# Optimization experiments

Hardware: AMD Instinct MI355X
Metric: run time of the kernel (lower is better)

Reference implementation:

```python
import jax, jax.numpy as jnp
import numpy as np

B, C1, C2, H, W = 4, 128, 256, 128, 128
K, S = 3, 1
N = K * K  # num sampled points = 9
BN_EPS = 1e-5


def setup_inputs() -> dict:
    key = jax.random.key(0)
    ks = jax.random.split(key, 8)
    x = jax.random.normal(ks[0], (B, C1, H, W), jnp.float32)
    # offset-prediction conv: 3x3, stride S, pad 1, out channels 2*N
    w_off = jax.random.normal(ks[1], (2 * N, C1, 3, 3), jnp.float32) * 0.01
    b_off = jnp.zeros((2 * N,), jnp.float32)
    # main conv over the N sampled points: equivalent to Conv2d(C1,C2,(N,1),stride=(N,1),bias=None)
    w_main = jax.random.normal(ks[2], (C2, C1, N), jnp.float32) * (1.0 / np.sqrt(C1 * N))
    bn_gamma = jax.random.uniform(ks[3], (C2,), jnp.float32, 0.5, 1.5)
    bn_beta = jax.random.normal(ks[4], (C2,), jnp.float32) * 0.1
    bn_mean = jax.random.normal(ks[5], (C2,), jnp.float32) * 0.1
    bn_var = jax.random.uniform(ks[6], (C2,), jnp.float32, 0.5, 1.5)
    return dict(x=x, w_off=w_off, b_off=b_off, w_main=w_main,
                bn_gamma=bn_gamma, bn_beta=bn_beta, bn_mean=bn_mean, bn_var=bn_var)


def _grid_pn():
    # base kernel sampling grid for N points: round(sqrt(N)) x base grid, values 0..base-1
    base = int(round(np.sqrt(N)))
    px, py = np.meshgrid(np.arange(base), np.arange(base), indexing='ij')
    return jnp.asarray(px.reshape(-1), jnp.float32), jnp.asarray(py.reshape(-1), jnp.float32)


def _akconv_forward(x, w_off, b_off, w_main, bn_gamma, bn_beta, bn_mean, bn_var):
    # offset prediction: (b, 2N, h, w)
    offset = jax.lax.conv_general_dilated(
        x, w_off, (S, S), ((1, 1), (1, 1)),
        dimension_numbers=('NCHW', 'OIHW', 'NCHW')) + b_off[None, :, None, None]
    b, _, h, w = offset.shape
    off_x = offset[:, :N].transpose(0, 2, 3, 1)   # (b,h,w,N) row offsets
    off_y = offset[:, N:].transpose(0, 2, 3, 1)   # (b,h,w,N) col offsets
    pn_x, pn_y = _grid_pn()
    p0_x = (jnp.arange(h, dtype=jnp.float32) * S)[None, :, None, None]
    p0_y = (jnp.arange(w, dtype=jnp.float32) * S)[None, None, :, None]
    px = jnp.clip(off_x + pn_x[None, None, None, :] + p0_x, 0.0, H - 1.0)
    py = jnp.clip(off_y + pn_y[None, None, None, :] + p0_y, 0.0, W - 1.0)
    x0 = jnp.clip(jnp.floor(px), 0.0, H - 1.0)
    y0 = jnp.clip(jnp.floor(py), 0.0, W - 1.0)
    x1 = jnp.clip(x0 + 1.0, 0.0, H - 1.0)
    y1 = jnp.clip(y0 + 1.0, 0.0, W - 1.0)
    # bilinear weights (official AKConv formulation)
    g_lt = (1.0 + (x0 - px)) * (1.0 + (y0 - py))
    g_rb = (1.0 - (x1 - px)) * (1.0 - (y1 - py))
    g_lb = (1.0 + (x0 - px)) * (1.0 - (y1 - py))
    g_rt = (1.0 - (x1 - px)) * (1.0 + (y0 - py))
    xf = x.reshape(b, C1, H * W)

    def gather(qx, qy):
        idx = (qx * W + qy).astype(jnp.int32).reshape(b, 1, h * w * N)
        g = jnp.take_along_axis(xf, jnp.broadcast_to(idx, (b, C1, h * w * N)), axis=2)
        return g.reshape(b, C1, h, w, N)

    # fused bilinear combine: (b, C1, h, w, N)
    x_off = (g_lt[:, None] * gather(x0, y0)
             + g_rb[:, None] * gather(x1, y1)
             + g_lb[:, None] * gather(x0, y1)
             + g_rt[:, None] * gather(x1, y0))
    # main conv over sampled points == Conv2d(kernel=(N,1), stride=(N,1)) on rearranged tensor
    out = jnp.einsum('bchwn,ocn->bohw', x_off, w_main)
    # inference-mode BatchNorm
    inv = bn_gamma / jnp.sqrt(bn_var + BN_EPS)
    out = out * inv[None, :, None, None] + (bn_beta - bn_mean * inv)[None, :, None, None]
    # wrapper SiLU activation
    return jax.nn.silu(out)


def reference(x, w_off, b_off, w_main, bn_gamma, bn_beta, bn_mean, bn_var):
    return _akconv_forward(x, w_off, b_off, w_main, bn_gamma, bn_beta, bn_mean, bn_var)
```

## Files before the change

kernel.cpp:

```cpp
#include <hip/hip_runtime.h>
#include <math.h>

typedef __attribute__((ext_vector_type(8))) short short8;
typedef __attribute__((ext_vector_type(4))) float f32x4;
typedef __attribute__((ext_vector_type(2))) float f32x2;
typedef __attribute__((ext_vector_type(4))) uint  uint4v;
typedef __attribute__((ext_vector_type(4))) int   int4v;

#define BB  4
#define C1  128
#define C2  256
#define HH  128
#define WW  128
#define NPT 9
#define HWN (HH*WW)

#define XT_OFF    0ull
#define WB3_OFF   16777216ull
#define BN_OFF    (WB3_OFF + 589824ull)
#define OFFP_OFF  (BN_OFF + 2048ull)
#define PART_OFF  (OFFP_OFF + 4718592ull)
#define WS_FUSED_NEED (PART_OFF + 18874368ull)

#define NB_OFF  (4 * BB * HH)
#define NB_TR   (BB * 4 * HH * 2)
#define NB_PREP 1153

__device__ __forceinline__ ushort f2bf(float f) {
  uint u = __builtin_bit_cast(uint, f);
  u += 0x7FFFu + ((u >> 16) & 1u);
  return (ushort)(u >> 16);
}
__device__ __forceinline__ float u2f(uint u) {
  return __builtin_bit_cast(float, u);
}

__global__ __launch_bounds__(256) void stage1(
    const float* __restrict__ x, const float* __restrict__ b_off,
    const float* __restrict__ w_off, const float* __restrict__ w_main,
    const float* __restrict__ g, const float* __restrict__ be,
    const float* __restrict__ mu, const float* __restrict__ var,
    ushort* ws_u, float* ws_f, float* __restrict__ part) {
  __shared__ __align__(16) ushort tile[32][68];
  int blk = blockIdx.x;
  int tid = threadIdx.x;

  if (blk < NB_OFF) {
    int cg = blk & 3, bh = blk >> 2;
    int h = bh & 127, b = bh >> 7;
    int w = tid & 127, q = tid >> 7;
    int qu = __builtin_amdgcn_readfirstlane(q);
    int quoff = qu * 9;
    const float* xb = x + ((size_t)b * C1 + cg * 32) * HWN;

    f32x2 acc2[9];
    float accs[9];
#pragma unroll
    for (int i = 0; i < 9; ++i) {
      acc2[i] = (f32x2)0.0f;
      accs[i] = (cg == 0) ? b_off[quoff + i] : 0.f;
    }

    int hc0 = (h >= 1) ? h - 1 : 0, hc2 = (h < 127) ? h + 1 : 127;
    int wc0 = (w >= 1) ? w - 1 : 0, wc2 = (w < 127) ? w + 1 : 127;
    bool vh0 = (h >= 1), vh2 = (h < 127);
    bool vw0 = (w >= 1), vw2 = (w < 127);
    int o[9];
    o[0] = hc0 * 128 + wc0; o[1] = hc0 * 128 + w; o[2] = hc0 * 128 + wc2;
    o[3] = h   * 128 + wc0; o[4] = h   * 128 + w; o[5] = h   * 128 + wc2;
    o[6] = hc2 * 128 + wc0; o[7] = hc2 * 128 + w; o[8] = hc2 * 128 + wc2;
    bool vm[9];
    vm[0] = vh0 && vw0; vm[1] = vh0; vm[2] = vh0 && vw2;
    vm[3] = vw0;        vm[4] = true; vm[5] = vw2;
    vm[6] = vh2 && vw0; vm[7] = vh2; vm[8] = vh2 && vw2;

    for (int ci = 0; ci < 32; ++ci) {
      int c = cg * 32 + ci;
      const float* xc = xb + (size_t)ci * HWN;
      float xv[9];
#pragma unroll
      for (int k = 0; k < 9; ++k) {
        float rr = xc[o[k]];
        xv[k] = vm[k] ? rr : 0.f;
      }
      f32x2 xp0 = {xv[0], xv[1]}, xp1 = {xv[2], xv[3]};
      f32x2 xp2 = {xv[4], xv[5]}, xp3 = {xv[6], xv[7]};
      float x8 = xv[8];
#pragma unroll
      for (int i = 0; i < 9; ++i) {
        const float* wp = w_off + ((size_t)(quoff + i) * C1 + c) * 9;
        f32x2 w01 = {wp[0], wp[1]}, w23 = {wp[2], wp[3]};
        f32x2 w45 = {wp[4], wp[5]}, w67 = {wp[6], wp[7]};
        acc2[i] = xp0 * w01 + acc2[i];
        acc2[i] = xp1 * w23 + acc2[i];
        acc2[i] = xp2 * w45 + acc2[i];
        acc2[i] = xp3 * w67 + acc2[i];
        accs[i] = fmaf(x8, wp[8], accs[i]);
      }
    }
    int pos = (b * HH + h) * WW + w;
#pragma unroll
    for (int i = 0; i < 9; ++i)
      part[(size_t)(cg * 18 + quoff + i) * 65536 + pos] = acc2[i][0] + acc2[i][1] + accs[i];

  } else if (blk < NB_OFF + NB_TR) {
    int bid = blk - NB_OFF;
    int wt = bid & 1, h = (bid >> 1) & 127, cb = (bid >> 8) & 3, b = bid >> 10;
    int c0 = cb * 32, w0 = wt * 64;
    int wl = tid & 63, rr = tid >> 6;
#pragma unroll
    for (int it = 0; it < 8; ++it) {
      int ci = it * 4 + rr;
      tile[ci][wl] = f2bf(x[(((size_t)b * C1 + c0 + ci) * HWN) + h * WW + w0 + wl]);
    }
    __syncthreads();
    int wl2 = tid >> 2, cg = tid & 3;
    short8 pk;
#pragma unroll
    for (int k = 0; k < 8; ++k) pk[k] = (short)tile[cg * 8 + k][wl2];
    *(short8*)(ws_u + XT_OFF / 2 +
               (((size_t)(b * HH + h) * WW + w0 + wl2) * C1 + c0 + cg * 8)) = pk;

  } else {
    int t = (blk - NB_OFF - NB_TR) * 256 + tid;
    if (t < C1 * NPT * C2) {
      int j = t & 7, lane = (t >> 3) & 63, kc = (t >> 9) & 3;
      int ob = (t >> 11) & 15, n = t >> 15;
      int o = ob * 16 + (lane & 15);
      int c = kc * 32 + (lane >> 4) * 8 + j;
      ws_u[WB3_OFF / 2 + t] = f2bf(w_main[(o * C1 + c) * NPT + n]);
    } else {
      int o = t - C1 * NPT * C2;
      float inv = g[o] * rsqrtf(var[o] + 1e-5f);
      ws_f[BN_OFF / 4 + o] = inv;
      ws_f[BN_OFF / 4 + 256 + o] = be[o] - mu[o] * inv;
    }
  }
}

__global__ __launch_bounds__(256) void off_reduce_soa(
    const float* __restrict__ part, float* __restrict__ ws_f) {
  int e = blockIdx.x * 256 + threadIdx.x;
  int oc = e >> 16, pos = e & 65535;
  float s = part[(size_t)oc * 65536 + pos]
          + part[(size_t)(18 + oc) * 65536 + pos]
          + part[(size_t)(36 + oc) * 65536 + pos]
          + part[(size_t)(54 + oc) * 65536 + pos];
  ws_f[OFFP_OFF / 4 + (size_t)oc * 65536 + pos] = s;
}

#define ALDS_STRIDE 136
__global__ __launch_bounds__(1024, 8) void akconv_main_mfma16(
    const ushort* ws_u, const float* ws_f, float* out, int fused) {
  __shared__ __align__(16) int4v sidx[576];
  __shared__ __align__(16) f32x4 swgt[576];
  __shared__ __align__(16) ushort alds[2][64 * ALDS_STRIDE];

  int tid = threadIdx.x;
  int blk = blockIdx.x;
  int xcd = blk & 7, idx = blk >> 3;
  int b  = xcd >> 1;
  int h  = ((xcd & 1) << 6) + (idx >> 1);
  int wt = idx & 1;
  int w0 = wt * 64;

  if (tid < 576) {
    int n = tid >> 6, wl = tid & 63;
    int pos = (b * HH + h) * WW + w0 + wl;
    float ox, oy;
    if (fused) {
      const float* pp = ws_f + PART_OFF / 4;
      ox = pp[(size_t)n * 65536 + pos]
         + pp[(size_t)(18 + n) * 65536 + pos]
         + pp[(size_t)(36 + n) * 65536 + pos]
         + pp[(size_t)(54 + n) * 65536 + pos];
      oy = pp[(size_t)(9 + n) * 65536 + pos]
         + pp[(size_t)(27 + n) * 65536 + pos]
         + pp[(size_t)(45 + n) * 65536 + pos]
         + pp[(size_t)(63 + n) * 65536 + pos];
    } else {
      const float* offp = ws_f + OFFP_OFF / 4;
      ox = offp[(size_t)n * 65536 + pos];
      oy = offp[(size_t)(9 + n) * 65536 + pos];
    }
    float px = ox + (float)(n / 3) + (float)h;
    float py = oy + (float)(n - (n / 3) * 3) + (float)(w0 + wl);
    px = fminf(fmaxf(px, 0.f), 127.f);
    py = fminf(fmaxf(py, 0.f), 127.f);
    float x0 = floorf(px), y0 = floorf(py);
    float x1 = fminf(x0 + 1.f, 127.f), y1 = fminf(y0 + 1.f, 127.f);
    f32x4 g;
    g[0] = (1.f + (x0 - px)) * (1.f + (y0 - py));
    g[1] = (1.f - (x1 - px)) * (1.f - (y1 - py));
    g[2] = (1.f + (x0 - px)) * (1.f - (y1 - py));
    g[3] = (1.f - (x1 - px)) * (1.f + (y0 - py));
    int ix0 = (int)x0, iy0 = (int)y0, ix1 = (int)x1, iy1 = (int)y1;
    int4v iv;
    iv[0] = (ix0 * WW + iy0) << 8;
    iv[1] = (ix1 * WW + iy1) << 8;
    iv[2] = (ix0 * WW + iy1) << 8;
    iv[3] = (ix1 * WW + iy0) << 8;
    sidx[tid] = iv;
    swgt[tid] = g;
  }

  const char* xTb = (const char*)ws_u + (size_t)b * (HWN * 256);
  const ushort* wB3 = ws_u + WB3_OFF / 2;
  int lane = tid & 63, r = lane & 15, kg = lane >> 4;
  int wv = __builtin_amdgcn_readfirstlane(tid >> 6);

  int p   = tid >> 4;
  int oct = tid & 15;
  int coff = oct * 16;
  int wr = p * ALDS_STRIDE + oct * 8;

  f32x4 acc[4];
#pragma unroll
  for (int mi = 0; mi < 4; ++mi) acc[mi] = (f32x4)0.0f;

  __syncthreads();

  uint4v gv[4];
  f32x4 gw;

#define GLOAD(nn)                                                       \
  {                                                                     \
    int e = (nn) * 64 + p;                                              \
    int4v iv = sidx[e];                                                 \
    gw = swgt[e];                                                       \
    gv[0] = *(const uint4v*)(xTb + iv[0] + coff);                       \
    gv[1] = *(const uint4v*)(xTb + iv[1] + coff);                       \
    gv[2] = *(const uint4v*)(xTb + iv[2] + coff);                       \
    gv[3] = *(const uint4v*)(xTb + iv[3] + coff);                       \
  }

#define GCOMBINE(bufb)                                                  \
  {                                                                     \
    uint4v pkv;                                                         \
    _Pragma("unroll")                                                   \
    for (int jj = 0; jj < 4; ++jj) {                                    \
      float flo = gw[0] * u2f(gv[0][jj] << 16) + gw[1] * u2f(gv[1][jj] << 16) \
                + gw[2] * u2f(gv[2][jj] << 16) + gw[3] * u2f(gv[3][jj] << 16);\
      float fhi = gw[0] * u2f(gv[0][jj] & 0xffff0000u)                  \
                + gw[1] * u2f(gv[1][jj] & 0xffff0000u)                  \
                + gw[2] * u2f(gv[2][jj] & 0xffff0000u)                  \
                + gw[3] * u2f(gv[3][jj] & 0xffff0000u);                 \
      uint upk;                                                         \
      asm("v_cvt_pk_bf16_f32 %0, %1, %2" : "=v"(upk) : "v"(flo), "v"(fhi)); \
      pkv[jj] = upk;                                                    \
    }                                                                   \
    *(uint4v*)(&alds[bufb][wr]) = pkv;                                  \
  }

  GLOAD(0);
  GCOMBINE(0);
  __syncthreads();

  for (int n = 0; n < 9; ++n) {
    int buf = n & 1;
    if (n < 8) GLOAD(n + 1);
#pragma unroll
    for (int kc = 0; kc < 4; ++kc) {
      short8 bfrag = *(const short8*)(wB3 +
          (((size_t)(n * 16 + wv) * 4 + kc) * 64 + lane) * 8);
#pragma unroll
      for (int mi = 0; mi < 4; ++mi) {
        short8 a = *(const short8*)(&alds[buf][(mi * 16 + r) * ALDS_STRIDE + (kc * 4 + kg) * 8]);
        acc[mi] = __builtin_amdgcn_mfma_f32_16x16x32_bf16(bfrag, a, acc[mi], 0, 0, 0);
      }
    }
    if (n < 8) GCOMBINE(buf ^ 1);
    __syncthreads();
  }
#undef GLOAD
#undef GCOMBINE

  const float* bnA = ws_f + BN_OFF / 4;
  const float* bnB = bnA + 256;
  int ob = wv * 16 + kg * 4;
#pragma unroll
  for (int j = 0; j < 4; ++j) {
    int o = ob + j;
    float sA = bnA[o], sB = bnB[o];
#pragma unroll
    for (int mi = 0; mi < 4; ++mi) {
      float v = acc[mi][j] * sA + sB;
      float sv = v / (1.f + __expf(-v));
      out[(((size_t)b * C2 + o) * HWN) + h * WW + w0 + mi * 16 + r] = sv;
    }
  }
}

extern "C" void kernel_launch(void* const* d_in, const int* in_sizes, int n_in,
                              void* d_out, int out_size, void* d_ws, size_t ws_size,
                              hipStream_t stream) {
  const float* x        = (const float*)d_in[0];
  const float* w_off    = (const float*)d_in[1];
  const float* b_off    = (const float*)d_in[2];
  const float* w_main   = (const float*)d_in[3];
  const float* bn_gamma = (const float*)d_in[4];
  const float* bn_beta  = (const float*)d_in[5];
  const float* bn_mean  = (const float*)d_in[6];
  const float* bn_var   = (const float*)d_in[7];
  ushort* ws_u = (ushort*)d_ws;
  float*  ws_f = (float*)d_ws;
  float*  out  = (float*)d_out;

  int fused = (ws_size >= WS_FUSED_NEED) ? 1 : 0;
  float* part_dst = fused ? (ws_f + PART_OFF / 4) : out;

  stage1<<<NB_OFF + NB_TR + NB_PREP, 256, 0, stream>>>(
      x, b_off, w_off, w_main, bn_gamma, bn_beta, bn_mean, bn_var,
      ws_u, ws_f, part_dst);
  if (!fused) {
    off_reduce_soa<<<(18 * 65536) / 256, 256, 0, stream>>>(out, ws_f);
  }
  akconv_main_mfma16<<<BB * HH * 2, 1024, 0, stream>>>(ws_u, ws_f, out, fused);
}
```

Measured before the change: 132.0 us.

## Shrink main kernel tile to 32 pixels with 8 waves covering two output blocks

```diff
diff --git a/kernel.cpp b/kernel.cpp
--- a/kernel.cpp
+++ b/kernel.cpp
@@ -150,22 +150,22 @@
 }
 
 #define ALDS_STRIDE 136
-__global__ __launch_bounds__(1024, 8) void akconv_main_mfma16(
+__global__ __launch_bounds__(512, 4) void akconv_main_w8(
     const ushort* ws_u, const float* ws_f, float* out, int fused) {
-  __shared__ __align__(16) int4v sidx[576];
-  __shared__ __align__(16) f32x4 swgt[576];
-  __shared__ __align__(16) ushort alds[2][64 * ALDS_STRIDE];
+  __shared__ __align__(16) int4v sidx[288];
+  __shared__ __align__(16) f32x4 swgt[288];
+  __shared__ __align__(16) ushort alds[2][32 * ALDS_STRIDE];
 
   int tid = threadIdx.x;
   int blk = blockIdx.x;
   int xcd = blk & 7, idx = blk >> 3;
   int b  = xcd >> 1;
-  int h  = ((xcd & 1) << 6) + (idx >> 1);
-  int wt = idx & 1;
-  int w0 = wt * 64;
-
-  if (tid < 576) {
-    int n = tid >> 6, wl = tid & 63;
+  int h  = ((xcd & 1) << 6) + (idx >> 2);
+  int wt = idx & 3;
+  int w0 = wt * 32;
+
+  if (tid < 288) {
+    int n = tid >> 5, wl = tid & 31;
     int pos = (b * HH + h) * WW + w0 + wl;
     float ox, oy;
     if (fused) {
@@ -189,11 +189,11 @@
     py = fminf(fmaxf(py, 0.f), 127.f);
     float x0 = floorf(px), y0 = floorf(py);
     float x1 = fminf(x0 + 1.f, 127.f), y1 = fminf(y0 + 1.f, 127.f);
-    f32x4 g;
-    g[0] = (1.f + (x0 - px)) * (1.f + (y0 - py));
-    g[1] = (1.f - (x1 - px)) * (1.f - (y1 - py));
-    g[2] = (1.f + (x0 - px)) * (1.f - (y1 - py));
-    g[3] = (1.f - (x1 - px)) * (1.f + (y0 - py));
+    f32x4 gg;
+    gg[0] = (1.f + (x0 - px)) * (1.f + (y0 - py));
+    gg[1] = (1.f - (x1 - px)) * (1.f - (y1 - py));
+    gg[2] = (1.f + (x0 - px)) * (1.f - (y1 - py));
+    gg[3] = (1.f - (x1 - px)) * (1.f + (y0 - py));
     int ix0 = (int)x0, iy0 = (int)y0, ix1 = (int)x1, iy1 = (int)y1;
     int4v iv;
     iv[0] = (ix0 * WW + iy0) << 8;
@@ -201,22 +201,24 @@
     iv[2] = (ix0 * WW + iy1) << 8;
     iv[3] = (ix1 * WW + iy0) << 8;
     sidx[tid] = iv;
-    swgt[tid] = g;
+    swgt[tid] = gg;
   }
 
   const char* xTb = (const char*)ws_u + (size_t)b * (HWN * 256);
   const ushort* wB3 = ws_u + WB3_OFF / 2;
   int lane = tid & 63, r = lane & 15, kg = lane >> 4;
-  int wv = __builtin_amdgcn_readfirstlane(tid >> 6);
+  int wv2 = __builtin_amdgcn_readfirstlane(tid >> 6) * 2;
 
   int p   = tid >> 4;
   int oct = tid & 15;
   int coff = oct * 16;
   int wr = p * ALDS_STRIDE + oct * 8;
 
-  f32x4 acc[4];
-#pragma unroll
-  for (int mi = 0; mi < 4; ++mi) acc[mi] = (f32x4)0.0f;
+  f32x4 acc[2][2];
+#pragma unroll
+  for (int mi = 0; mi < 2; ++mi)
+#pragma unroll
+    for (int oi = 0; oi < 2; ++oi) acc[mi][oi] = (f32x4)0.0f;
 
   __syncthreads();
 
@@ -225,7 +227,7 @@
 
 #define GLOAD(nn)                                                       \
   {                                                                     \
-    int e = (nn) * 64 + p;                                              \
+    int e = (nn) * 32 + p;                                              \
     int4v iv = sidx[e];                                                 \
     gw = swgt[e];                                                       \
     gv[0] = *(const uint4v*)(xTb + iv[0] + coff);                       \
@@ -236,17 +238,21 @@
 
 #define GCOMBINE(bufb)                                                  \
   {                                                                     \
+    f32x2 gd0 = {gw[0], gw[0]}, gd1 = {gw[1], gw[1]};                   \
+    f32x2 gd2 = {gw[2], gw[2]}, gd3 = {gw[3], gw[3]};                   \
     uint4v pkv;                                                         \
     _Pragma("unroll")                                                   \
     for (int jj = 0; jj < 4; ++jj) {                                    \
-      float flo = gw[0] * u2f(gv[0][jj] << 16) + gw[1] * u2f(gv[1][jj] << 16) \
-                + gw[2] * u2f(gv[2][jj] << 16) + gw[3] * u2f(gv[3][jj] << 16);\
-      float fhi = gw[0] * u2f(gv[0][jj] & 0xffff0000u)                  \
-                + gw[1] * u2f(gv[1][jj] & 0xffff0000u)                  \
-                + gw[2] * u2f(gv[2][jj] & 0xffff0000u)                  \
-                + gw[3] * u2f(gv[3][jj] & 0xffff0000u);                 \
+      f32x2 a0 = {u2f(gv[0][jj] << 16), u2f(gv[0][jj] & 0xffff0000u)};  \
+      f32x2 a1 = {u2f(gv[1][jj] << 16), u2f(gv[1][jj] & 0xffff0000u)};  \
+      f32x2 a2 = {u2f(gv[2][jj] << 16), u2f(gv[2][jj] & 0xffff0000u)};  \
+      f32x2 a3 = {u2f(gv[3][jj] << 16), u2f(gv[3][jj] & 0xffff0000u)};  \
+      f32x2 s = a0 * gd0;                                               \
+      s = a1 * gd1 + s;                                                 \
+      s = a2 * gd2 + s;                                                 \
+      s = a3 * gd3 + s;                                                 \
       uint upk;                                                         \
-      asm("v_cvt_pk_bf16_f32 %0, %1, %2" : "=v"(upk) : "v"(flo), "v"(fhi)); \
+      asm("v_cvt_pk_bf16_f32 %0, %1, %2" : "=v"(upk) : "v"(s[0]), "v"(s[1])); \
       pkv[jj] = upk;                                                    \
     }                                                                   \
     *(uint4v*)(&alds[bufb][wr]) = pkv;                                  \
@@ -261,12 +267,15 @@
     if (n < 8) GLOAD(n + 1);
 #pragma unroll
     for (int kc = 0; kc < 4; ++kc) {
-      short8 bfrag = *(const short8*)(wB3 +
-          (((size_t)(n * 16 + wv) * 4 + kc) * 64 + lane) * 8);
-#pragma unroll
-      for (int mi = 0; mi < 4; ++mi) {
+      short8 b0 = *(const short8*)(wB3 +
+          (((size_t)(n * 16 + wv2) * 4 + kc) * 64 + lane) * 8);
+      short8 b1 = *(const short8*)(wB3 +
+          (((size_t)(n * 16 + wv2 + 1) * 4 + kc) * 64 + lane) * 8);
+#pragma unroll
+      for (int mi = 0; mi < 2; ++mi) {
         short8 a = *(const short8*)(&alds[buf][(mi * 16 + r) * ALDS_STRIDE + (kc * 4 + kg) * 8]);
-        acc[mi] = __builtin_amdgcn_mfma_f32_16x16x32_bf16(bfrag, a, acc[mi], 0, 0, 0);
+        acc[mi][0] = __builtin_amdgcn_mfma_f32_16x16x32_bf16(b0, a, acc[mi][0], 0, 0, 0);
+        acc[mi][1] = __builtin_amdgcn_mfma_f32_16x16x32_bf16(b1, a, acc[mi][1], 0, 0, 0);
       }
     }
     if (n < 8) GCOMBINE(buf ^ 1);
@@ -277,16 +286,18 @@
 
   const float* bnA = ws_f + BN_OFF / 4;
   const float* bnB = bnA + 256;
-  int ob = wv * 16 + kg * 4;
-#pragma unroll
-  for (int j = 0; j < 4; ++j) {
-    int o = ob + j;
-    float sA = bnA[o], sB = bnB[o];
-#pragma unroll
-    for (int mi = 0; mi < 4; ++mi) {
-      float v = acc[mi][j] * sA + sB;
-      float sv = v / (1.f + __expf(-v));
-      out[(((size_t)b * C2 + o) * HWN) + h * WW + w0 + mi * 16 + r] = sv;
+#pragma unroll
+  for (int oi = 0; oi < 2; ++oi) {
+#pragma unroll
+    for (int j = 0; j < 4; ++j) {
+      int o = (wv2 + oi) * 16 + kg * 4 + j;
+      float sA = bnA[o], sB = bnB[o];
+#pragma unroll
+      for (int mi = 0; mi < 2; ++mi) {
+        float v = acc[mi][oi][j] * sA + sB;
+        float sv = v / (1.f + __expf(-v));
+        out[(((size_t)b * C2 + o) * HWN) + h * WW + w0 + mi * 16 + r] = sv;
+      }
     }
   }
 }
@@ -315,5 +326,5 @@
   if (!fused) {
     off_reduce_soa<<<(18 * 65536) / 256, 256, 0, stream>>>(out, ws_f);
   }
-  akconv_main_mfma16<<<BB * HH * 2, 1024, 0, stream>>>(ws_u, ws_f, out, fused);
-}
+  akconv_main_w8<<<BB * HH * 4, 512, 0, stream>>>(ws_u, ws_f, out, fused);
+}
```

New measurement: 136.0 us. +3.1%, slower.
